# Optimization experiments

Hardware: AMD Instinct MI355X
Metric: run time of the kernel (lower is better)

Reference implementation:

```python
import jax, jax.numpy as jnp
import numpy as np
import math

G, B, L, C = 4, 4, 512, 768
NH, DH = 12, 64  # num heads, head dim; NH*DH == C

def setup_inputs() -> dict:
    key = jax.random.key(0)
    ks = jax.random.split(key, 8)
    s = 0.02
    return {
        "hidden_states": jax.random.normal(ks[0], (G, B, L, C), jnp.float32),
        "attention_mask": jnp.zeros((G, B, 1, 1, L), jnp.float32),
        "query_weight": jax.random.normal(ks[1], (G, C, C), jnp.float32) * s,
        "query_bias": jax.random.normal(ks[2], (G, 1, C), jnp.float32) * s,
        "key_weight": jax.random.normal(ks[3], (G, C, C), jnp.float32) * s,
        "key_bias": jax.random.normal(ks[4], (G, 1, C), jnp.float32) * s,
        "value_weight": jax.random.normal(ks[5], (G, C, C), jnp.float32) * s,
        "value_bias": jax.random.normal(ks[6], (G, 1, C), jnp.float32) * s,
    }

def _heads(x):
    # [g, b*l, c] -> [g, b, nh, l, dh]
    return x.reshape(G, B, L, NH, DH).transpose(0, 1, 3, 2, 4)

def reference(hidden_states, attention_mask, query_weight, query_bias,
              key_weight, key_bias, value_weight, value_bias):
    hs = hidden_states.reshape(G, B * L, C)
    q = _heads(jnp.einsum('gtc,gcd->gtd', hs, query_weight) + query_bias)
    k = _heads(jnp.einsum('gtc,gcd->gtd', hs, key_weight) + key_bias)
    v = _heads(jnp.einsum('gtc,gcd->gtd', hs, value_weight) + value_bias)
    scale = 1.0 / math.sqrt(DH)
    scores = jnp.einsum('gbhld,gbhmd->gbhlm', q, k) * scale + attention_mask
    probs = jax.nn.softmax(scores, axis=-1)  # dropout prob = 0.0 -> identity
    ctx = jnp.einsum('gbhlm,gbhmd->gbhld', probs, v)
    ctx = ctx.transpose(0, 1, 3, 2, 4).reshape(G, B, L, NH * DH)
    return ctx
```

## Files before the change

kernel.cpp:

```cpp
#include <hip/hip_runtime.h>

#define G_ 4
#define B_ 4
#define L_ 512
#define C_ 768
#define NH_ 12
#define DH_ 64
#define T_ 2048

typedef __bf16 bf16x8 __attribute__((ext_vector_type(8)));
typedef float f32x4 __attribute__((ext_vector_type(4)));
typedef unsigned int u32x4 __attribute__((ext_vector_type(4)));
typedef unsigned short u16;
typedef unsigned short u16x4 __attribute__((ext_vector_type(4)));

__device__ __forceinline__ u16 f2bf(float x) {
    unsigned u = __builtin_bit_cast(unsigned, x);
    u = (u + 0x7FFFu + ((u >> 16) & 1u)) >> 16;
    return (u16)u;
}

__global__ void k_convert(const float* __restrict__ in, u16* __restrict__ out, int n4) {
    int i = blockIdx.x * blockDim.x + threadIdx.x;
    if (i >= n4) return;
    float4 v = reinterpret_cast<const float4*>(in)[i];
    u16x4 o;
    o.x = f2bf(v.x); o.y = f2bf(v.y); o.z = f2bf(v.z); o.w = f2bf(v.w);
    reinterpret_cast<u16x4*>(out)[i] = o;
}

__global__ void k_transpose(const float* __restrict__ wq, const float* __restrict__ wk,
                            const float* __restrict__ wv, u16* __restrict__ wt) {
    __shared__ u16 tile[32][33];
    int qkv = blockIdx.z >> 2, g = blockIdx.z & 3;
    const float* W = (qkv == 0 ? wq : qkv == 1 ? wk : wv) + g * (C_ * C_);
    u16* O = wt + blockIdx.z * (C_ * C_);
    int d0 = blockIdx.x * 32, c0 = blockIdx.y * 32;
    int tx = threadIdx.x, ty = threadIdx.y;
#pragma unroll
    for (int j = 0; j < 4; j++)
        tile[ty + 8 * j][tx] = f2bf(W[(c0 + ty + 8 * j) * C_ + d0 + tx]);
    __syncthreads();
#pragma unroll
    for (int j = 0; j < 4; j++)
        O[(d0 + ty + 8 * j) * C_ + c0 + tx] = tile[tx][ty + 8 * j];
}

#define BM 128
#define BN 128
#define BK 64
#define LDK 72

__global__ __launch_bounds__(256) void k_qkv_gemm(
    const u16* __restrict__ hsb, const u16* __restrict__ wt,
    const float* __restrict__ qb, const float* __restrict__ kb,
    const float* __restrict__ vb, u16* __restrict__ qkvout) {
    __shared__ u16 Asm[BM * LDK];
    __shared__ u16 Bsm[BN * LDK];
    int qkv = blockIdx.z >> 2, g = blockIdx.z & 3;
    int n0 = blockIdx.x * BN, m0 = blockIdx.y * BM;
    const u16* Ag = hsb + g * (T_ * C_);
    const u16* Bg = wt + blockIdx.z * (C_ * C_);
    const float* bias = (qkv == 0 ? qb : qkv == 1 ? kb : vb) + g * C_;
    u16* Og = qkvout + qkv * (G_ * T_ * C_) + g * (T_ * C_);

    int tid = threadIdx.x;
    int lane = tid & 63, w = tid >> 6;
    int wm = (w >> 1) * 64, wn = (w & 1) * 64;
    int l15 = lane & 15, l4 = lane >> 4;

    f32x4 acc[4][4];
#pragma unroll
    for (int a = 0; a < 4; a++)
#pragma unroll
        for (int b = 0; b < 4; b++) acc[a][b] = (f32x4){0.f, 0.f, 0.f, 0.f};

    for (int k0 = 0; k0 < C_; k0 += BK) {
#pragma unroll
        for (int it = 0; it < 4; it++) {
            int ch = tid + it * 256;
            int r = ch >> 3, c8 = ch & 7;
            u32x4 a = *reinterpret_cast<const u32x4*>(Ag + (m0 + r) * C_ + k0 + c8 * 8);
            *reinterpret_cast<u32x4*>(&Asm[r * LDK + c8 * 8]) = a;
            u32x4 b = *reinterpret_cast<const u32x4*>(Bg + (n0 + r) * C_ + k0 + c8 * 8);
            *reinterpret_cast<u32x4*>(&Bsm[r * LDK + c8 * 8]) = b;
        }
        __syncthreads();
#pragma unroll
        for (int kk = 0; kk < 2; kk++) {
            bf16x8 af[4], bfr[4];
#pragma unroll
            for (int mi = 0; mi < 4; mi++)
                af[mi] = __builtin_bit_cast(bf16x8, *reinterpret_cast<const u32x4*>(
                             &Asm[(wm + mi * 16 + l15) * LDK + kk * 32 + l4 * 8]));
#pragma unroll
            for (int ni = 0; ni < 4; ni++)
                bfr[ni] = __builtin_bit_cast(bf16x8, *reinterpret_cast<const u32x4*>(
                              &Bsm[(wn + ni * 16 + l15) * LDK + kk * 32 + l4 * 8]));
#pragma unroll
            for (int mi = 0; mi < 4; mi++)
#pragma unroll
                for (int ni = 0; ni < 4; ni++)
                    acc[mi][ni] = __builtin_amdgcn_mfma_f32_16x16x32_bf16(
                        af[mi], bfr[ni], acc[mi][ni], 0, 0, 0);
        }
        __syncthreads();
    }
#pragma unroll
    for (int ni = 0; ni < 4; ni++) {
        int col = n0 + wn + ni * 16 + l15;
        float bv = bias[col];
#pragma unroll
        for (int mi = 0; mi < 4; mi++) {
#pragma unroll
            for (int i = 0; i < 4; i++) {
                int row = m0 + wm + mi * 16 + l4 * 4 + i;
                Og[row * C_ + col] = f2bf(acc[mi][ni][i] + bv);
            }
        }
    }
}

#define LDA 72
#define SCALE 0.125f

__global__ __launch_bounds__(256) void k_attn(
    const u16* __restrict__ qkv, const float* __restrict__ mask,
    float* __restrict__ out) {
    __shared__ u16 Ksm[64 * LDA];
    __shared__ u16 Vsm[64 * LDA];
    __shared__ u16 Psm[64 * LDA];
    __shared__ float msk[L_];

    int qt = blockIdx.x, h = blockIdx.y, gb = blockIdx.z;
    int g = gb >> 2, b = gb & 3;
    int q0 = qt * 64;
    int tid = threadIdx.x, lane = tid & 63, w = tid >> 6;
    int l15 = lane & 15, l4 = lane >> 4;

    const int QKVSZ = G_ * T_ * C_;
    const u16* Qg = qkv + g * (T_ * C_) + (b * L_) * C_ + h * DH_;
    const u16* Kg = qkv + QKVSZ + g * (T_ * C_) + (b * L_) * C_ + h * DH_;
    const u16* Vg = qkv + 2 * QKVSZ + g * (T_ * C_) + (b * L_) * C_ + h * DH_;

    for (int i = tid; i < L_; i += 256) msk[i] = mask[(g * B_ + b) * L_ + i];

    bf16x8 qf[2];
#pragma unroll
    for (int kk = 0; kk < 2; kk++)
        qf[kk] = __builtin_bit_cast(bf16x8, *reinterpret_cast<const u32x4*>(
                     Qg + (q0 + w * 16 + l15) * C_ + kk * 32 + l4 * 8));

    float mrun[4], lrun[4];
    f32x4 accO[4];
#pragma unroll
    for (int i = 0; i < 4; i++) { mrun[i] = -1e30f; lrun[i] = 0.f; }
#pragma unroll
    for (int df = 0; df < 4; df++) accO[df] = (f32x4){0.f, 0.f, 0.f, 0.f};

    int r = tid >> 2, c8a = tid & 3;
    for (int kt = 0; kt < 8; kt++) {
        int krow0 = kt * 64;
        __syncthreads();
#pragma unroll
        for (int half = 0; half < 2; half++) {
            int c8 = c8a + half * 4;
            u32x4 kv = *reinterpret_cast<const u32x4*>(Kg + (krow0 + r) * C_ + c8 * 8);
            *reinterpret_cast<u32x4*>(&Ksm[r * LDA + c8 * 8]) = kv;
            u32x4 vv = *reinterpret_cast<const u32x4*>(Vg + (krow0 + r) * C_ + c8 * 8);
            union { u32x4 q; u16 u[8]; } uu; uu.q = vv;
#pragma unroll
            for (int j = 0; j < 8; j++)
                Vsm[(c8 * 8 + j) * LDA + r] = uu.u[j];
        }
        __syncthreads();

        f32x4 s[4];
#pragma unroll
        for (int nf = 0; nf < 4; nf++) s[nf] = (f32x4){0.f, 0.f, 0.f, 0.f};
#pragma unroll
        for (int kk = 0; kk < 2; kk++) {
#pragma unroll
            for (int nf = 0; nf < 4; nf++) {
                bf16x8 kf = __builtin_bit_cast(bf16x8, *reinterpret_cast<const u32x4*>(
                                &Ksm[(nf * 16 + l15) * LDA + kk * 32 + l4 * 8]));
                s[nf] = __builtin_amdgcn_mfma_f32_16x16x32_bf16(qf[kk], kf, s[nf], 0, 0, 0);
            }
        }

        float mv[4];
#pragma unroll
        for (int nf = 0; nf < 4; nf++) mv[nf] = msk[krow0 + nf * 16 + l15];

        float p[4][4];
#pragma unroll
        for (int i = 0; i < 4; i++) {
            float sv[4];
#pragma unroll
            for (int nf = 0; nf < 4; nf++) sv[nf] = fmaf(s[nf][i], SCALE, mv[nf]);
            float mx = fmaxf(fmaxf(sv[0], sv[1]), fmaxf(sv[2], sv[3]));
            mx = fmaxf(mx, __shfl_xor(mx, 1));
            mx = fmaxf(mx, __shfl_xor(mx, 2));
            mx = fmaxf(mx, __shfl_xor(mx, 4));
            mx = fmaxf(mx, __shfl_xor(mx, 8));
            float mn = fmaxf(mrun[i], mx);
            float alpha = __expf(mrun[i] - mn);
            mrun[i] = mn;
            float rs = 0.f;
#pragma unroll
            for (int nf = 0; nf < 4; nf++) { p[nf][i] = __expf(sv[nf] - mn); rs += p[nf][i]; }
            rs += __shfl_xor(rs, 1);
            rs += __shfl_xor(rs, 2);
            rs += __shfl_xor(rs, 4);
            rs += __shfl_xor(rs, 8);
            lrun[i] = lrun[i] * alpha + rs;
#pragma unroll
            for (int df = 0; df < 4; df++) accO[df][i] *= alpha;
        }

#pragma unroll
        for (int nf = 0; nf < 4; nf++)
#pragma unroll
            for (int i = 0; i < 4; i++)
                Psm[(w * 16 + l4 * 4 + i) * LDA + nf * 16 + l15] = f2bf(p[nf][i]);

#pragma unroll
        for (int kk = 0; kk < 2; kk++) {
            bf16x8 pf = __builtin_bit_cast(bf16x8, *reinterpret_cast<const u32x4*>(
                            &Psm[(w * 16 + l15) * LDA + kk * 32 + l4 * 8]));
#pragma unroll
            for (int df = 0; df < 4; df++) {
                bf16x8 vf = __builtin_bit_cast(bf16x8, *reinterpret_cast<const u32x4*>(
                                &Vsm[(df * 16 + l15) * LDA + kk * 32 + l4 * 8]));
                accO[df] = __builtin_amdgcn_mfma_f32_16x16x32_bf16(pf, vf, accO[df], 0, 0, 0);
            }
        }
    }

#pragma unroll
    for (int i = 0; i < 4; i++) {
        float inv = 1.0f / lrun[i];
        int row = q0 + w * 16 + l4 * 4 + i;
#pragma unroll
        for (int df = 0; df < 4; df++)
            out[((g * B_ + b) * L_ + row) * C_ + h * DH_ + df * 16 + l15] =
                accO[df][i] * inv;
    }
}

extern "C" void kernel_launch(void* const* d_in, const int* in_sizes, int n_in,
                              void* d_out, int out_size, void* d_ws, size_t ws_size,
                              hipStream_t stream) {
    (void)in_sizes; (void)n_in; (void)out_size; (void)ws_size;
    const float* hs = (const float*)d_in[0];
    const float* mask = (const float*)d_in[1];
    const float* qw = (const float*)d_in[2];
    const float* qb = (const float*)d_in[3];
    const float* kw = (const float*)d_in[4];
    const float* kb = (const float*)d_in[5];
    const float* vw = (const float*)d_in[6];
    const float* vb = (const float*)d_in[7];
    float* out = (float*)d_out;

    char* ws = (char*)d_ws;
    const size_t OFF_WT = (size_t)G_ * T_ * C_ * 2;
    const size_t OFF_QKV = OFF_WT + (size_t)3 * G_ * C_ * C_ * 2;
    u16* hsb = (u16*)ws;
    u16* wt = (u16*)(ws + OFF_WT);
    u16* qkvb = (u16*)(ws + OFF_QKV);

    int n4 = (G_ * T_ * C_) / 4;
    k_convert<<<(n4 + 255) / 256, 256, 0, stream>>>(hs, hsb, n4);
    k_transpose<<<dim3(C_ / 32, C_ / 32, 12), dim3(32, 8), 0, stream>>>(qw, kw, vw, wt);
    k_qkv_gemm<<<dim3(C_ / BN, T_ / BM, 12), 256, 0, stream>>>(hsb, wt, qb, kb, vb, qkvb);
    k_attn<<<dim3(L_ / 64, NH_, G_ * B_), 256, 0, stream>>>(qkvb, mask, out);
}
```

Before: 220.5 us.

## Use direct global-to-LDS loads with XOR swizzle and pre-transposed V

New measurement: 279.2 us. 1.27x slower.

```diff
diff --git a/kernel.cpp b/kernel.cpp
--- a/kernel.cpp
+++ b/kernel.cpp
@@ -18,6 +18,13 @@
     unsigned u = __builtin_bit_cast(unsigned, x);
     u = (u + 0x7FFFu + ((u >> 16) & 1u)) >> 16;
     return (u16)u;
+}
+
+__device__ __forceinline__ void gload16(const void* g, unsigned lds_off) {
+    __builtin_amdgcn_global_load_lds(
+        (const __attribute__((address_space(1))) unsigned int*)(uintptr_t)g,
+        (__attribute__((address_space(3))) unsigned int*)(uintptr_t)(size_t)lds_off,
+        16, 0, 0);
 }
 
 __global__ void k_convert(const float* __restrict__ in, u16* __restrict__ out, int n4) {
@@ -49,14 +56,13 @@
 #define BM 128
 #define BN 128
 #define BK 64
-#define LDK 72
 
 __global__ __launch_bounds__(256) void k_qkv_gemm(
     const u16* __restrict__ hsb, const u16* __restrict__ wt,
     const float* __restrict__ qb, const float* __restrict__ kb,
-    const float* __restrict__ vb, u16* __restrict__ qkvout) {
-    __shared__ u16 Asm[BM * LDK];
-    __shared__ u16 Bsm[BN * LDK];
+    const float* __restrict__ vb, u16* __restrict__ qkvout, u16* __restrict__ vtout) {
+    __shared__ u16 Asm[BM * BK];
+    __shared__ u16 Bsm[BN * BK];
     int qkv = blockIdx.z >> 2, g = blockIdx.z & 3;
     int n0 = blockIdx.x * BN, m0 = blockIdx.y * BM;
     const u16* Ag = hsb + g * (T_ * C_);
@@ -64,10 +70,11 @@
     const float* bias = (qkv == 0 ? qb : qkv == 1 ? kb : vb) + g * C_;
     u16* Og = qkvout + qkv * (G_ * T_ * C_) + g * (T_ * C_);
 
-    int tid = threadIdx.x;
-    int lane = tid & 63, w = tid >> 6;
+    int tid = threadIdx.x, lane = tid & 63, w = tid >> 6;
     int wm = (w >> 1) * 64, wn = (w & 1) * 64;
     int l15 = lane & 15, l4 = lane >> 4;
+    unsigned abase = (unsigned)(uintptr_t)Asm;
+    unsigned bbase = (unsigned)(uintptr_t)Bsm;
 
     f32x4 acc[4][4];
 #pragma unroll
@@ -78,25 +85,31 @@
     for (int k0 = 0; k0 < C_; k0 += BK) {
 #pragma unroll
         for (int it = 0; it < 4; it++) {
-            int ch = tid + it * 256;
-            int r = ch >> 3, c8 = ch & 7;
-            u32x4 a = *reinterpret_cast<const u32x4*>(Ag + (m0 + r) * C_ + k0 + c8 * 8);
-            *reinterpret_cast<u32x4*>(&Asm[r * LDK + c8 * 8]) = a;
-            u32x4 b = *reinterpret_cast<const u32x4*>(Bg + (n0 + r) * C_ + k0 + c8 * 8);
-            *reinterpret_cast<u32x4*>(&Bsm[r * LDK + c8 * 8]) = b;
+            int s = it * 256 + tid;
+            int v = s ^ ((s >> 3) & 7);
+            int r = v >> 3, c8 = v & 7;
+            unsigned lb = (unsigned)((it * 256 + w * 64) * 16);
+            gload16(Ag + (m0 + r) * C_ + k0 + c8 * 8, abase + lb);
+            gload16(Bg + (n0 + r) * C_ + k0 + c8 * 8, bbase + lb);
         }
         __syncthreads();
+        const char* Ac = (const char*)Asm;
+        const char* Bc = (const char*)Bsm;
 #pragma unroll
         for (int kk = 0; kk < 2; kk++) {
             bf16x8 af[4], bfr[4];
 #pragma unroll
-            for (int mi = 0; mi < 4; mi++)
-                af[mi] = __builtin_bit_cast(bf16x8, *reinterpret_cast<const u32x4*>(
-                             &Asm[(wm + mi * 16 + l15) * LDK + kk * 32 + l4 * 8]));
-#pragma unroll
-            for (int ni = 0; ni < 4; ni++)
-                bfr[ni] = __builtin_bit_cast(bf16x8, *reinterpret_cast<const u32x4*>(
-                              &Bsm[(wn + ni * 16 + l15) * LDK + kk * 32 + l4 * 8]));
+            for (int mi = 0; mi < 4; mi++) {
+                int row = wm + mi * 16 + l15;
+                unsigned off = (unsigned)(row * 128 + kk * 64 + l4 * 16) ^ (unsigned)((row & 7) << 4);
+                af[mi] = __builtin_bit_cast(bf16x8, *reinterpret_cast<const u32x4*>(Ac + off));
+            }
+#pragma unroll
+            for (int ni = 0; ni < 4; ni++) {
+                int row = wn + ni * 16 + l15;
+                unsigned off = (unsigned)(row * 128 + kk * 64 + l4 * 16) ^ (unsigned)((row & 7) << 4);
+                bfr[ni] = __builtin_bit_cast(bf16x8, *reinterpret_cast<const u32x4*>(Bc + off));
+            }
 #pragma unroll
             for (int mi = 0; mi < 4; mi++)
 #pragma unroll
@@ -106,33 +119,53 @@
         }
         __syncthreads();
     }
-#pragma unroll
-    for (int ni = 0; ni < 4; ni++) {
-        int col = n0 + wn + ni * 16 + l15;
-        float bv = bias[col];
-#pragma unroll
-        for (int mi = 0; mi < 4; mi++) {
-#pragma unroll
-            for (int i = 0; i < 4; i++) {
-                int row = m0 + wm + mi * 16 + l4 * 4 + i;
-                Og[row * C_ + col] = f2bf(acc[mi][ni][i] + bv);
-            }
-        }
-    }
-}
-
-#define LDA 72
+    if (qkv == 2) {
+#pragma unroll
+        for (int ni = 0; ni < 4; ni++) {
+            int col = n0 + wn + ni * 16 + l15;
+            int h = col >> 6, d = col & 63;
+            float bv = bias[col];
+#pragma unroll
+            for (int mi = 0; mi < 4; mi++) {
+#pragma unroll
+                for (int i = 0; i < 4; i++) {
+                    int row = m0 + wm + mi * 16 + l4 * 4 + i;
+                    int bb = row >> 9, l = row & 511;
+                    vtout[(((g * B_ + bb) * NH_ + h) * DH_ + d) * L_ + l] =
+                        f2bf(acc[mi][ni][i] + bv);
+                }
+            }
+        }
+    } else {
+#pragma unroll
+        for (int ni = 0; ni < 4; ni++) {
+            int col = n0 + wn + ni * 16 + l15;
+            float bv = bias[col];
+#pragma unroll
+            for (int mi = 0; mi < 4; mi++) {
+#pragma unroll
+                for (int i = 0; i < 4; i++) {
+                    int row = m0 + wm + mi * 16 + l4 * 4 + i;
+                    Og[row * C_ + col] = f2bf(acc[mi][ni][i] + bv);
+                }
+            }
+        }
+    }
+}
+
 #define SCALE 0.125f
+#define LDP 72
 
 __global__ __launch_bounds__(256) void k_attn(
-    const u16* __restrict__ qkv, const float* __restrict__ mask,
-    float* __restrict__ out) {
-    __shared__ u16 Ksm[64 * LDA];
-    __shared__ u16 Vsm[64 * LDA];
-    __shared__ u16 Psm[64 * LDA];
+    const u16* __restrict__ qkv, const u16* __restrict__ vt,
+    const float* __restrict__ mask, float* __restrict__ out) {
+    __shared__ u16 Psm[64 * LDP];
     __shared__ float msk[L_];
 
-    int qt = blockIdx.x, h = blockIdx.y, gb = blockIdx.z;
+    int bid = blockIdx.x;
+    int head = bid % (G_ * B_ * NH_);
+    int qt = bid / (G_ * B_ * NH_);
+    int h = head % NH_, gb = head / NH_;
     int g = gb >> 2, b = gb & 3;
     int q0 = qt * 64;
     int tid = threadIdx.x, lane = tid & 63, w = tid >> 6;
@@ -140,10 +173,11 @@
 
     const int QKVSZ = G_ * T_ * C_;
     const u16* Qg = qkv + g * (T_ * C_) + (b * L_) * C_ + h * DH_;
-    const u16* Kg = qkv + QKVSZ + g * (T_ * C_) + (b * L_) * C_ + h * DH_;
-    const u16* Vg = qkv + 2 * QKVSZ + g * (T_ * C_) + (b * L_) * C_ + h * DH_;
-
-    for (int i = tid; i < L_; i += 256) msk[i] = mask[(g * B_ + b) * L_ + i];
+    const u16* Kg = Qg + QKVSZ;
+    const u16* VtH = vt + (size_t)(gb * NH_ + h) * (DH_ * L_);
+
+    for (int i = tid; i < L_; i += 256) msk[i] = mask[gb * L_ + i];
+    __syncthreads();
 
     bf16x8 qf[2];
 #pragma unroll
@@ -158,33 +192,19 @@
 #pragma unroll
     for (int df = 0; df < 4; df++) accO[df] = (f32x4){0.f, 0.f, 0.f, 0.f};
 
-    int r = tid >> 2, c8a = tid & 3;
     for (int kt = 0; kt < 8; kt++) {
         int krow0 = kt * 64;
-        __syncthreads();
-#pragma unroll
-        for (int half = 0; half < 2; half++) {
-            int c8 = c8a + half * 4;
-            u32x4 kv = *reinterpret_cast<const u32x4*>(Kg + (krow0 + r) * C_ + c8 * 8);
-            *reinterpret_cast<u32x4*>(&Ksm[r * LDA + c8 * 8]) = kv;
-            u32x4 vv = *reinterpret_cast<const u32x4*>(Vg + (krow0 + r) * C_ + c8 * 8);
-            union { u32x4 q; u16 u[8]; } uu; uu.q = vv;
-#pragma unroll
-            for (int j = 0; j < 8; j++)
-                Vsm[(c8 * 8 + j) * LDA + r] = uu.u[j];
-        }
-        __syncthreads();
-
-        f32x4 s[4];
-#pragma unroll
-        for (int nf = 0; nf < 4; nf++) s[nf] = (f32x4){0.f, 0.f, 0.f, 0.f};
+
+        f32x4 s4[4];
+#pragma unroll
+        for (int nf = 0; nf < 4; nf++) s4[nf] = (f32x4){0.f, 0.f, 0.f, 0.f};
 #pragma unroll
         for (int kk = 0; kk < 2; kk++) {
 #pragma unroll
             for (int nf = 0; nf < 4; nf++) {
                 bf16x8 kf = __builtin_bit_cast(bf16x8, *reinterpret_cast<const u32x4*>(
-                                &Ksm[(nf * 16 + l15) * LDA + kk * 32 + l4 * 8]));
-                s[nf] = __builtin_amdgcn_mfma_f32_16x16x32_bf16(qf[kk], kf, s[nf], 0, 0, 0);
+                    Kg + (krow0 + nf * 16 + l15) * C_ + kk * 32 + l4 * 8));
+                s4[nf] = __builtin_amdgcn_mfma_f32_16x16x32_bf16(qf[kk], kf, s4[nf], 0, 0, 0);
             }
         }
 
@@ -197,7 +217,7 @@
         for (int i = 0; i < 4; i++) {
             float sv[4];
 #pragma unroll
-            for (int nf = 0; nf < 4; nf++) sv[nf] = fmaf(s[nf][i], SCALE, mv[nf]);
+            for (int nf = 0; nf < 4; nf++) sv[nf] = fmaf(s4[nf][i], SCALE, mv[nf]);
             float mx = fmaxf(fmaxf(sv[0], sv[1]), fmaxf(sv[2], sv[3]));
             mx = fmaxf(mx, __shfl_xor(mx, 1));
             mx = fmaxf(mx, __shfl_xor(mx, 2));
@@ -222,16 +242,16 @@
         for (int nf = 0; nf < 4; nf++)
 #pragma unroll
             for (int i = 0; i < 4; i++)
-                Psm[(w * 16 + l4 * 4 + i) * LDA + nf * 16 + l15] = f2bf(p[nf][i]);
+                Psm[(w * 16 + l4 * 4 + i) * LDP + nf * 16 + l15] = f2bf(p[nf][i]);
 
 #pragma unroll
         for (int kk = 0; kk < 2; kk++) {
             bf16x8 pf = __builtin_bit_cast(bf16x8, *reinterpret_cast<const u32x4*>(
-                            &Psm[(w * 16 + l15) * LDA + kk * 32 + l4 * 8]));
+                            &Psm[(w * 16 + l15) * LDP + kk * 32 + l4 * 8]));
 #pragma unroll
             for (int df = 0; df < 4; df++) {
                 bf16x8 vf = __builtin_bit_cast(bf16x8, *reinterpret_cast<const u32x4*>(
-                                &Vsm[(df * 16 + l15) * LDA + kk * 32 + l4 * 8]));
+                    VtH + (df * 16 + l15) * L_ + krow0 + kk * 32 + l4 * 8));
                 accO[df] = __builtin_amdgcn_mfma_f32_16x16x32_bf16(pf, vf, accO[df], 0, 0, 0);
             }
         }
@@ -268,10 +288,11 @@
     u16* hsb = (u16*)ws;
     u16* wt = (u16*)(ws + OFF_WT);
     u16* qkvb = (u16*)(ws + OFF_QKV);
+    u16* vtb = qkvb + 2 * (size_t)G_ * T_ * C_;
 
     int n4 = (G_ * T_ * C_) / 4;
     k_convert<<<(n4 + 255) / 256, 256, 0, stream>>>(hs, hsb, n4);
     k_transpose<<<dim3(C_ / 32, C_ / 32, 12), dim3(32, 8), 0, stream>>>(qw, kw, vw, wt);
-    k_qkv_gemm<<<dim3(C_ / BN, T_ / BM, 12), 256, 0, stream>>>(hsb, wt, qb, kb, vb, qkvb);
-    k_attn<<<dim3(L_ / 64, NH_, G_ * B_), 256, 0, stream>>>(qkvb, mask, out);
-}
+    k_qkv_gemm<<<dim3(C_ / BN, T_ / BM, 12), 256, 0, stream>>>(hsb, wt, qb, kb, vb, qkvb, vtb);
+    k_attn<<<dim3(L_ / 64 * NH_ * G_ * B_), 256, 0, stream>>>(qkvb, vtb, mask, out);
+}
```
